# Kernel optimization log

Measured on AMD Instinct MI355X. Metric: run time of the kernel, lower is better.

Reference implementation:

```python
import jax, jax.numpy as jnp
import numpy as np

B, S, D, H, HD = 2, 2048, 2048, 16, 128  # batch, seq, embed, heads, head_dim


def setup_inputs() -> dict:
    key = jax.random.key(0)
    k0, k1, k2 = jax.random.split(key, 3)
    hidden_states = jax.random.normal(k0, (B, S, D), dtype=jnp.float32)
    # fused QKV projection: [D, H*HD + 2*HD] (multi-query: single shared K and V head)
    W_attn = jax.random.normal(k1, (D, H * HD + 2 * HD), dtype=jnp.float32) * 0.02
    b_attn = jnp.zeros((H * HD + 2 * HD,), dtype=jnp.float32)
    W_proj = jax.random.normal(k2, (D, D), dtype=jnp.float32) * 0.02
    b_proj = jnp.zeros((D,), dtype=jnp.float32)
    # causal mask, broadcastable to (B, Q, H, K); True = attend
    attention_mask = jnp.tril(jnp.ones((S, S), dtype=bool))[None, :, None, :]
    return {
        "hidden_states": hidden_states,
        "W_attn": W_attn,
        "b_attn": b_attn,
        "W_proj": W_proj,
        "b_proj": b_proj,
        "attention_mask": attention_mask,
    }


def reference(hidden_states, W_attn, b_attn, W_proj, b_proj, attention_mask):
    # fused QKV, then split into Q (H heads) and shared K/V (multi-query)
    qkv = hidden_states @ W_attn + b_attn          # (B, S, H*HD + 2*HD)
    q = qkv[..., : H * HD].reshape(B, S, H, HD)    # (B, Q, H, hd)
    key_t = qkv[..., H * HD : H * HD + HD]         # (B, K, hd) shared K head
    value = qkv[..., H * HD + HD :]                # (B, K, hd) shared V head

    # dtype == softmax_dtype (fp32) -> upcast=False, unscale=1
    scale_factor = 1.0 / (HD ** 0.5)               # scale_attn_weights
    attn_weights = jnp.einsum("bqhd,bkd->bqhk", q, key_t) * scale_factor
    mask_value = jnp.finfo(jnp.float32).min
    attn_weights = jnp.where(attention_mask, attn_weights, mask_value)
    attn_weights = jax.nn.softmax(attn_weights, axis=-1)

    attn_output = jnp.einsum("bqhk,bkd->bqhd", attn_weights, value)
    attn_output = attn_output.reshape(B, S, H * HD)
    return attn_output @ W_proj + b_proj           # (B, S, D)
```

## Files before the change

kernel.cpp:

```cpp
#include <hip/hip_runtime.h>
#include <math.h>

constexpr int cB  = 2;
constexpr int cS  = 2048;
constexpr int cD  = 2048;
constexpr int cH  = 16;
constexpr int cHD = 128;
constexpr int cNQKV = cH * cHD + 2 * cHD;

typedef __attribute__((ext_vector_type(8))) short bf16x8;
typedef __attribute__((ext_vector_type(4))) float f32x4;

__device__ __forceinline__ short f2bf(float f) {
    union { float f; unsigned u; } v; v.f = f;
    unsigned r = (v.u + 0x7FFFu + ((v.u >> 16) & 1u)) >> 16;
    return (short)r;
}

typedef __attribute__((address_space(3))) void lds_t;
typedef const __attribute__((address_space(1))) void gbl_t;
__device__ __forceinline__ void gld16(const void* g, void* l) {
    __builtin_amdgcn_global_load_lds((gbl_t*)g, (lds_t*)l, 16, 0, 0);
}

__global__ __launch_bounds__(256) void conv_bf16(
    const float* __restrict__ src, short* __restrict__ dst)
{
    size_t i = ((size_t)blockIdx.x * 256 + threadIdx.x) * 8;
    float4 a = *(const float4*)(src + i);
    float4 b = *(const float4*)(src + i + 4);
    bf16x8 o;
    o[0] = f2bf(a.x); o[1] = f2bf(a.y); o[2] = f2bf(a.z); o[3] = f2bf(a.w);
    o[4] = f2bf(b.x); o[5] = f2bf(b.y); o[6] = f2bf(b.z); o[7] = f2bf(b.w);
    *(bf16x8*)(dst + i) = o;
}

__global__ __launch_bounds__(256) void transpose_bf16(
    const float* __restrict__ src, short* __restrict__ dst, int K, int N)
{
    __shared__ short t[32][33];
    const int n0 = blockIdx.x * 32, k0 = blockIdx.y * 32;
    const int x = threadIdx.x & 31, y = threadIdx.x >> 5;
#pragma unroll
    for (int i = 0; i < 4; ++i)
        t[y + 8 * i][x] = f2bf(src[(size_t)(k0 + y + 8 * i) * N + n0 + x]);
    __syncthreads();
#pragma unroll
    for (int i = 0; i < 4; ++i)
        dst[(size_t)(n0 + y + 8 * i) * K + k0 + x] = t[x][y + 8 * i];
}

template<bool BF16_OUT>
__global__ __launch_bounds__(256) void gemm_mfma(
    const short* __restrict__ A, const short* __restrict__ Bt,
    const float* __restrict__ bias, void* __restrict__ Cout,
    int M, int N, int K, float qscale, int qcols)
{
    __shared__ short As[128 * 32];
    __shared__ short Bs[128 * 32];

    const int tid = threadIdx.x;
    const int lane = tid & 63, n16 = lane & 15, quad = lane >> 4;
    const int wave = tid >> 6, wm = wave >> 1, wn = wave & 1;
    const int m0 = blockIdx.y * 128, n0 = blockIdx.x * 128;

    f32x4 acc[4][4];
#pragma unroll
    for (int i = 0; i < 4; ++i)
#pragma unroll
        for (int j = 0; j < 4; ++j) acc[i][j] = 0.0f;

    const int s0 = tid, s1 = tid + 256;
    const short* Ag0 = A  + (size_t)(m0 + (s0 >> 2)) * K + (s0 & 3) * 8;
    const short* Ag1 = A  + (size_t)(m0 + (s1 >> 2)) * K + (s1 & 3) * 8;
    const short* Bg0 = Bt + (size_t)(n0 + (s0 >> 2)) * K + (s0 & 3) * 8;
    const short* Bg1 = Bt + (size_t)(n0 + (s1 >> 2)) * K + (s1 & 3) * 8;

    for (int k0 = 0; k0 < K; k0 += 32) {
        gld16(Ag0 + k0, &As[s0 * 8]);
        gld16(Ag1 + k0, &As[s1 * 8]);
        gld16(Bg0 + k0, &Bs[s0 * 8]);
        gld16(Bg1 + k0, &Bs[s1 * 8]);
        __syncthreads();
        bf16x8 af[4], bfr[4];
#pragma unroll
        for (int mt = 0; mt < 4; ++mt)
            af[mt] = *(const bf16x8*)&As[(wm * 64 + mt * 16 + n16) * 32 + quad * 8];
#pragma unroll
        for (int nt = 0; nt < 4; ++nt)
            bfr[nt] = *(const bf16x8*)&Bs[(wn * 64 + nt * 16 + n16) * 32 + quad * 8];
#pragma unroll
        for (int mt = 0; mt < 4; ++mt)
#pragma unroll
            for (int nt = 0; nt < 4; ++nt)
                acc[mt][nt] = __builtin_amdgcn_mfma_f32_16x16x32_bf16(
                    af[mt], bfr[nt], acc[mt][nt], 0, 0, 0);
        __syncthreads();
    }

#pragma unroll
    for (int nt = 0; nt < 4; ++nt) {
        const int col = n0 + wn * 64 + nt * 16 + n16;
        const float bv = bias[col];
        const float sc = (col < qcols) ? qscale : 1.0f;
#pragma unroll
        for (int mt = 0; mt < 4; ++mt)
#pragma unroll
            for (int r = 0; r < 4; ++r) {
                const int row = m0 + wm * 64 + mt * 16 + quad * 4 + r;
                const float v = (acc[mt][nt][r] + bv) * sc;
                if (BF16_OUT) ((short*)Cout)[(size_t)row * N + col] = f2bf(v);
                else          ((float*)Cout)[(size_t)row * N + col] = v;
            }
    }
}

__global__ __launch_bounds__(256) void prep_v(
    const short* __restrict__ qkvb, short* __restrict__ Vt)
{
    const int b  = blockIdx.y;
    const int k0 = blockIdx.x * 64;
    const int t  = threadIdx.x;
#pragma unroll
    for (int i = 0; i < 32; ++i) {
        int idx = i * 256 + t;
        int hd = idx >> 6, key = idx & 63;
        Vt[((size_t)b * cHD + hd) * cS + k0 + key] =
            qkvb[((size_t)(b * cS + k0 + key)) * cNQKV + cH * cHD + cHD + hd];
    }
}

__global__ __launch_bounds__(256) void attn_mfma(
    const short* __restrict__ qkvb, const short* __restrict__ Vt,
    short* __restrict__ out)
{
    const int tid  = threadIdx.x;
    const int wave = tid >> 6;
    const int lane = tid & 63;
    const int n16  = lane & 15;
    const int quad = lane >> 4;
    const int qt = (int)gridDim.x - 1 - (int)blockIdx.x;
    const int h  = blockIdx.y;
    const int b  = blockIdx.z;
    const int q0 = qt * 64 + wave * 16;

    __shared__ __align__(16) short Ks[8192];
    __shared__ __align__(16) short Vs[8192];
    __shared__ __align__(16) short Ps[4][16][72];

    const int part = lane & 3;
    const int krow = lane >> 2;

    bf16x8 qf[4];
    {
        const short* qbase = qkvb + ((size_t)(b * cS) + q0 + n16) * cNQKV + h * cHD + quad * 8;
#pragma unroll
        for (int ch = 0; ch < 4; ++ch) qf[ch] = *(const bf16x8*)(qbase + ch * 32);
    }

    f32x4 oc[8];
#pragma unroll
    for (int on = 0; on < 8; ++on) oc[on] = 0.0f;
    float lp[4] = {0.0f, 0.0f, 0.0f, 0.0f};

    const short* kglob = qkvb + (size_t)b * cS * cNQKV + cH * cHD;
    const short* vbase = Vt + (size_t)b * cHD * cS;
    const int nkt = qt + 1;

    for (int kt = 0; kt < nkt; ++kt) {
        const int k0 = kt * 64;

        __syncthreads();
        {
            const short* kr = kglob + (size_t)(k0 + wave * 16 + krow) * cNQKV + part * 8;
#pragma unroll
            for (int j = 0; j < 4; ++j)
                gld16(kr + j * 32, &Ks[(j * 4 + wave) * 512]);
        }
        {
#pragma unroll
            for (int j = 0; j < 4; ++j) {
                const int idx = j * 4 + wave;
                const int c2 = idx >> 3;
                const int hd = (idx & 7) * 16 + krow;
                gld16(vbase + (size_t)hd * cS + k0 + c2 * 32 + part * 8,
                      &Vs[idx * 512]);
            }
        }
        __syncthreads();

        f32x4 sc[4];
#pragma unroll
        for (int nt = 0; nt < 4; ++nt) sc[nt] = 0.0f;
#pragma unroll
        for (int nt = 0; nt < 4; ++nt) {
#pragma unroll
            for (int ch = 0; ch < 4; ++ch) {
                bf16x8 kf = *(const bf16x8*)&Ks[(ch * 64 + nt * 16 + n16) * 32 + quad * 8];
                sc[nt] = __builtin_amdgcn_mfma_f32_16x16x32_bf16(qf[ch], kf, sc[nt], 0, 0, 0);
            }
        }

        if (kt == nkt - 1) {
#pragma unroll
            for (int nt = 0; nt < 4; ++nt)
#pragma unroll
                for (int r = 0; r < 4; ++r) {
                    int row = q0 + quad * 4 + r;
                    int col = k0 + nt * 16 + n16;
                    if (col > row) sc[nt][r] = -1e30f;
                }
        }

#pragma unroll
        for (int r = 0; r < 4; ++r)
#pragma unroll
            for (int nt = 0; nt < 4; ++nt) {
                float p = __expf(sc[nt][r]);
                lp[r] += p;
                Ps[wave][quad * 4 + r][nt * 16 + n16] = f2bf(p);
            }

        bf16x8 pf0 = *(const bf16x8*)&Ps[wave][n16][quad * 8];
        bf16x8 pf1 = *(const bf16x8*)&Ps[wave][n16][32 + quad * 8];

#pragma unroll
        for (int on = 0; on < 8; ++on) {
            bf16x8 vf0 = *(const bf16x8*)&Vs[(on * 16 + n16) * 32 + quad * 8];
            bf16x8 vf1 = *(const bf16x8*)&Vs[(128 * 32) + (on * 16 + n16) * 32 + quad * 8];
            oc[on] = __builtin_amdgcn_mfma_f32_16x16x32_bf16(pf0, vf0, oc[on], 0, 0, 0);
            oc[on] = __builtin_amdgcn_mfma_f32_16x16x32_bf16(pf1, vf1, oc[on], 0, 0, 0);
        }
    }

    float inv[4];
#pragma unroll
    for (int r = 0; r < 4; ++r) {
        float t = lp[r];
        t += __shfl_xor(t, 1);
        t += __shfl_xor(t, 2);
        t += __shfl_xor(t, 4);
        t += __shfl_xor(t, 8);
        inv[r] = 1.0f / t;
    }
    short* obase = out + ((size_t)(b * cS) + q0) * cD + h * cHD;
#pragma unroll
    for (int on = 0; on < 8; ++on)
#pragma unroll
        for (int r = 0; r < 4; ++r)
            obase[(size_t)(quad * 4 + r) * cD + on * 16 + n16] = f2bf(oc[on][r] * inv[r]);
}

extern "C" void kernel_launch(void* const* d_in, const int* in_sizes, int n_in,
                              void* d_out, int out_size, void* d_ws, size_t ws_size,
                              hipStream_t stream)
{
    const float* hidden = (const float*)d_in[0];
    const float* W_attn = (const float*)d_in[1];
    const float* b_attn = (const float*)d_in[2];
    const float* W_proj = (const float*)d_in[3];
    const float* b_proj = (const float*)d_in[4];
    float* out = (float*)d_out;

    const int M = cB * cS;
    short* qkvb = (short*)d_ws;
    short* Ah   = qkvb + (size_t)M * cNQKV;
    short* Wb   = Ah   + (size_t)M * cD;
    short* Wpb  = Wb   + (size_t)cNQKV * cD;
    short* Vt   = Wpb  + (size_t)cD * cD;
    short* attno = Ah;

    const float scale = 0.088388347648318447f;

    conv_bf16<<<(size_t)M * cD / 2048, 256, 0, stream>>>(hidden, Ah);
    transpose_bf16<<<dim3(cNQKV / 32, cD / 32), 256, 0, stream>>>(W_attn, Wb, cD, cNQKV);
    transpose_bf16<<<dim3(cD / 32, cD / 32), 256, 0, stream>>>(W_proj, Wpb, cD, cD);

    gemm_mfma<true><<<dim3(cNQKV / 128, M / 128), 256, 0, stream>>>(
        Ah, Wb, b_attn, qkvb, M, cNQKV, cD, scale, cH * cHD);

    prep_v<<<dim3(cS / 64, cB), 256, 0, stream>>>(qkvb, Vt);

    attn_mfma<<<dim3(cS / 64, cH, cB), 256, 0, stream>>>(qkvb, Vt, attno);

    gemm_mfma<false><<<dim3(cD / 128, M / 128), 256, 0, stream>>>(
        attno, Wpb, b_proj, out, M, cD, cD, 1.0f, 0);
}
```

Before: 369.9 us.

## Double-buffer K/V tiles and pair causal query tiles per attention block

The attention kernel now keeps two LDS buffers for K and V and prefetches the next key tile while the current one is being computed. Each block now handles two query tiles, qt and 31-qt, so every block gets the same amount of causal work, and the grid is halved to match. MFMA sections are wrapped in s_setprio to raise wave priority during matrix work. The trade-off is double the K/V LDS per block, which can lower occupancy, and fewer blocks in flight.

```diff
diff --git a/kernel.cpp b/kernel.cpp
--- a/kernel.cpp
+++ b/kernel.cpp
@@ -139,116 +139,131 @@
     const int lane = tid & 63;
     const int n16  = lane & 15;
     const int quad = lane >> 4;
-    const int qt = (int)gridDim.x - 1 - (int)blockIdx.x;
     const int h  = blockIdx.y;
     const int b  = blockIdx.z;
-    const int q0 = qt * 64 + wave * 16;
-
-    __shared__ __align__(16) short Ks[8192];
-    __shared__ __align__(16) short Vs[8192];
+
+    __shared__ __align__(16) short Ks[2][8192];
+    __shared__ __align__(16) short Vs[2][8192];
     __shared__ __align__(16) short Ps[4][16][72];
 
     const int part = lane & 3;
     const int krow = lane >> 2;
 
-    bf16x8 qf[4];
-    {
-        const short* qbase = qkvb + ((size_t)(b * cS) + q0 + n16) * cNQKV + h * cHD + quad * 8;
-#pragma unroll
-        for (int ch = 0; ch < 4; ++ch) qf[ch] = *(const bf16x8*)(qbase + ch * 32);
-    }
-
-    f32x4 oc[8];
-#pragma unroll
-    for (int on = 0; on < 8; ++on) oc[on] = 0.0f;
-    float lp[4] = {0.0f, 0.0f, 0.0f, 0.0f};
-
     const short* kglob = qkvb + (size_t)b * cS * cNQKV + cH * cHD;
     const short* vbase = Vt + (size_t)b * cHD * cS;
-    const int nkt = qt + 1;
-
-    for (int kt = 0; kt < nkt; ++kt) {
-        const int k0 = kt * 64;
+
+    int cur = 0;
+
+    auto stage = [&](int buf, int k0) {
+        const short* kr = kglob + (size_t)(k0 + wave * 16 + krow) * cNQKV + part * 8;
+#pragma unroll
+        for (int j = 0; j < 4; ++j)
+            gld16(kr + j * 32, &Ks[buf][(j * 4 + wave) * 512]);
+#pragma unroll
+        for (int j = 0; j < 4; ++j) {
+            const int idx = j * 4 + wave;
+            const int c2 = idx >> 3;
+            const int hd = (idx & 7) * 16 + krow;
+            gld16(vbase + (size_t)hd * cS + k0 + c2 * 32 + part * 8,
+                  &Vs[buf][idx * 512]);
+        }
+    };
+
+#pragma unroll 1
+    for (int seg = 0; seg < 2; ++seg) {
+        const int qt = seg ? (int)blockIdx.x : 31 - (int)blockIdx.x;
+        const int q0 = qt * 64 + wave * 16;
+        const int nkt = qt + 1;
+
+        bf16x8 qf[4];
+        {
+            const short* qbase = qkvb + ((size_t)(b * cS) + q0 + n16) * cNQKV
+                               + h * cHD + quad * 8;
+#pragma unroll
+            for (int ch = 0; ch < 4; ++ch) qf[ch] = *(const bf16x8*)(qbase + ch * 32);
+        }
+
+        f32x4 oc[8];
+#pragma unroll
+        for (int on = 0; on < 8; ++on) oc[on] = 0.0f;
+        float lp[4] = {0.0f, 0.0f, 0.0f, 0.0f};
 
         __syncthreads();
-        {
-            const short* kr = kglob + (size_t)(k0 + wave * 16 + krow) * cNQKV + part * 8;
-#pragma unroll
-            for (int j = 0; j < 4; ++j)
-                gld16(kr + j * 32, &Ks[(j * 4 + wave) * 512]);
+        stage(cur, 0);
+
+#pragma unroll 1
+        for (int kt = 0; kt < nkt; ++kt) {
+            const int k0 = kt * 64;
+            __syncthreads();
+            if (kt + 1 < nkt) stage(cur ^ 1, k0 + 64);
+
+            f32x4 sc[4];
+#pragma unroll
+            for (int nt = 0; nt < 4; ++nt) sc[nt] = 0.0f;
+            __builtin_amdgcn_s_setprio(1);
+#pragma unroll
+            for (int nt = 0; nt < 4; ++nt) {
+#pragma unroll
+                for (int ch = 0; ch < 4; ++ch) {
+                    bf16x8 kf = *(const bf16x8*)&Ks[cur][(ch * 64 + nt * 16 + n16) * 32 + quad * 8];
+                    sc[nt] = __builtin_amdgcn_mfma_f32_16x16x32_bf16(qf[ch], kf, sc[nt], 0, 0, 0);
+                }
+            }
+            __builtin_amdgcn_s_setprio(0);
+
+            if (kt == nkt - 1) {
+#pragma unroll
+                for (int nt = 0; nt < 4; ++nt)
+#pragma unroll
+                    for (int r = 0; r < 4; ++r) {
+                        int row = q0 + quad * 4 + r;
+                        int col = k0 + nt * 16 + n16;
+                        if (col > row) sc[nt][r] = -1e30f;
+                    }
+            }
+
+#pragma unroll
+            for (int r = 0; r < 4; ++r)
+#pragma unroll
+                for (int nt = 0; nt < 4; ++nt) {
+                    float p = __expf(sc[nt][r]);
+                    lp[r] += p;
+                    Ps[wave][quad * 4 + r][nt * 16 + n16] = f2bf(p);
+                }
+
+            bf16x8 pf0 = *(const bf16x8*)&Ps[wave][n16][quad * 8];
+            bf16x8 pf1 = *(const bf16x8*)&Ps[wave][n16][32 + quad * 8];
+
+            __builtin_amdgcn_s_setprio(1);
+#pragma unroll
+            for (int on = 0; on < 8; ++on) {
+                bf16x8 vf0 = *(const bf16x8*)&Vs[cur][(on * 16 + n16) * 32 + quad * 8];
+                bf16x8 vf1 = *(const bf16x8*)&Vs[cur][(128 * 32) + (on * 16 + n16) * 32 + quad * 8];
+                oc[on] = __builtin_amdgcn_mfma_f32_16x16x32_bf16(pf0, vf0, oc[on], 0, 0, 0);
+                oc[on] = __builtin_amdgcn_mfma_f32_16x16x32_bf16(pf1, vf1, oc[on], 0, 0, 0);
+            }
+            __builtin_amdgcn_s_setprio(0);
+
+            cur ^= 1;
         }
-        {
-#pragma unroll
-            for (int j = 0; j < 4; ++j) {
-                const int idx = j * 4 + wave;
-                const int c2 = idx >> 3;
-                const int hd = (idx & 7) * 16 + krow;
-                gld16(vbase + (size_t)hd * cS + k0 + c2 * 32 + part * 8,
-                      &Vs[idx * 512]);
-            }
+
+        float inv[4];
+#pragma unroll
+        for (int r = 0; r < 4; ++r) {
+            float t = lp[r];
+            t += __shfl_xor(t, 1);
+            t += __shfl_xor(t, 2);
+            t += __shfl_xor(t, 4);
+            t += __shfl_xor(t, 8);
+            inv[r] = 1.0f / t;
         }
-        __syncthreads();
-
-        f32x4 sc[4];
-#pragma unroll
-        for (int nt = 0; nt < 4; ++nt) sc[nt] = 0.0f;
-#pragma unroll
-        for (int nt = 0; nt < 4; ++nt) {
-#pragma unroll
-            for (int ch = 0; ch < 4; ++ch) {
-                bf16x8 kf = *(const bf16x8*)&Ks[(ch * 64 + nt * 16 + n16) * 32 + quad * 8];
-                sc[nt] = __builtin_amdgcn_mfma_f32_16x16x32_bf16(qf[ch], kf, sc[nt], 0, 0, 0);
-            }
-        }
-
-        if (kt == nkt - 1) {
-#pragma unroll
-            for (int nt = 0; nt < 4; ++nt)
-#pragma unroll
-                for (int r = 0; r < 4; ++r) {
-                    int row = q0 + quad * 4 + r;
-                    int col = k0 + nt * 16 + n16;
-                    if (col > row) sc[nt][r] = -1e30f;
-                }
-        }
-
-#pragma unroll
-        for (int r = 0; r < 4; ++r)
-#pragma unroll
-            for (int nt = 0; nt < 4; ++nt) {
-                float p = __expf(sc[nt][r]);
-                lp[r] += p;
-                Ps[wave][quad * 4 + r][nt * 16 + n16] = f2bf(p);
-            }
-
-        bf16x8 pf0 = *(const bf16x8*)&Ps[wave][n16][quad * 8];
-        bf16x8 pf1 = *(const bf16x8*)&Ps[wave][n16][32 + quad * 8];
-
-#pragma unroll
-        for (int on = 0; on < 8; ++on) {
-            bf16x8 vf0 = *(const bf16x8*)&Vs[(on * 16 + n16) * 32 + quad * 8];
-            bf16x8 vf1 = *(const bf16x8*)&Vs[(128 * 32) + (on * 16 + n16) * 32 + quad * 8];
-            oc[on] = __builtin_amdgcn_mfma_f32_16x16x32_bf16(pf0, vf0, oc[on], 0, 0, 0);
-            oc[on] = __builtin_amdgcn_mfma_f32_16x16x32_bf16(pf1, vf1, oc[on], 0, 0, 0);
-        }
+        short* obase = out + ((size_t)(b * cS) + q0) * cD + h * cHD;
+#pragma unroll
+        for (int on = 0; on < 8; ++on)
+#pragma unroll
+            for (int r = 0; r < 4; ++r)
+                obase[(size_t)(quad * 4 + r) * cD + on * 16 + n16] = f2bf(oc[on][r] * inv[r]);
     }
-
-    float inv[4];
-#pragma unroll
-    for (int r = 0; r < 4; ++r) {
-        float t = lp[r];
-        t += __shfl_xor(t, 1);
-        t += __shfl_xor(t, 2);
-        t += __shfl_xor(t, 4);
-        t += __shfl_xor(t, 8);
-        inv[r] = 1.0f / t;
-    }
-    short* obase = out + ((size_t)(b * cS) + q0) * cD + h * cHD;
-#pragma unroll
-    for (int on = 0; on < 8; ++on)
-#pragma unroll
-        for (int r = 0; r < 4; ++r)
-            obase[(size_t)(quad * 4 + r) * cD + on * 16 + n16] = f2bf(oc[on][r] * inv[r]);
 }
 
 extern "C" void kernel_launch(void* const* d_in, const int* in_sizes, int n_in,
@@ -281,7 +296,7 @@
 
     prep_v<<<dim3(cS / 64, cB), 256, 0, stream>>>(qkvb, Vt);
 
-    attn_mfma<<<dim3(cS / 64, cH, cB), 256, 0, stream>>>(qkvb, Vt, attno);
+    attn_mfma<<<dim3(cS / 128, cH, cB), 256, 0, stream>>>(qkvb, Vt, attno);
 
     gemm_mfma<false><<<dim3(cD / 128, M / 128), 256, 0, stream>>>(
         attno, Wpb, b_proj, out, M, cD, cD, 1.0f, 0);
```

Result: faster. 323.9 us (-12.4%).
